# Performance work log

Hardware: AMD Instinct MI355X
Metric: run time of the kernel (lower is better)

The kernel has to match this reference:

```python
import jax, jax.numpy as jnp
import numpy as np

TEMPERATURE = 0.6
REPETITION_PENALTY = 1.2
VOCAB = 50257


def setup_inputs() -> dict:
    key = jax.random.key(0)
    k1, k2 = jax.random.split(key)
    logits = jax.random.normal(k1, (8, 64, VOCAB), dtype=jnp.float32)
    prev_tokens = jax.random.randint(k2, (64, 200), 0, VOCAB, dtype=jnp.int64)
    return {"logits": logits, "prev_tokens": prev_tokens}


def reference(logits, prev_tokens):
    # logits: [B, S, V]; prev_tokens: [S, P] token ids previously generated per sequence.
    B, S, V = logits.shape
    # set-semantics mask of penalized (seq, token) pairs; duplicate ids collapse to one.
    mask = jnp.zeros((S, V), dtype=bool).at[
        jnp.arange(S)[:, None], prev_tokens
    ].set(True)  # [S, V]
    # torch.all over dim 0: penalty multiplies if all batch logits negative, else divides.
    all_neg = jnp.all(logits < 0, axis=0, keepdims=True)  # [1, S, V]
    penalized = jnp.where(all_neg, logits * REPETITION_PENALTY, logits / REPETITION_PENALTY)
    logits = jnp.where(mask[None, :, :], penalized, logits)
    # Categorical(logits=x) -> probs = softmax(x); temperature scaling fused.
    return jax.nn.softmax(logits / TEMPERATURE, axis=-1)
```

## Files before the change

kernel.cpp:

```cpp
#include <hip/hip_runtime.h>
#include <math.h>

#define BB 8
#define SS 64
#define VV 50257
#define PP 200
#define NMASK 1571
#define NT 1024
#define ITER 13
constexpr float RP   = 1.2f;
constexpr float TINV = 1.0f / 0.6f;

__global__ __launch_bounds__(NT) void sch_fused_kernel(
        const float* __restrict__ logits,
        const int*   __restrict__ prev,
        float*       __restrict__ out) {
    __shared__ unsigned mask[NMASK];
    __shared__ float ss[16];
    __shared__ float bc_li;

    const int bs  = blockIdx.x;
    const int s   = bs & (SS - 1);
    const int tid = threadIdx.x;
    const float* row  = logits + (size_t)bs * VV;
    float*       orow = out    + (size_t)bs * VV;

    for (int i = tid; i < NMASK; i += NT) mask[i] = 0u;
    __syncthreads();

    float delta  = 0.0f;
    float eadj   = 0.0f;
    int   vtok   = -1;
    bool  winner = false;
    if (tid < PP) {
        vtok = prev[s * PP + tid];
        unsigned bit = 1u << (vtok & 31);
        unsigned old = atomicOr(&mask[vtok >> 5], bit);
        winner = (old & bit) == 0u;
        if (winner) {
            float lv[BB];
            bool all_neg = true;
            #pragma unroll
            for (int b = 0; b < BB; ++b) {
                lv[b] = logits[((size_t)(b * SS + s)) * VV + vtok];
                all_neg = all_neg && (lv[b] < 0.0f);
            }
            const float myraw = lv[bs >> 6];
            const float adj   = all_neg ? myraw * RP : myraw / RP;
            eadj  = __expf(adj * TINV);
            delta = eadj - __expf(myraw * TINV);
        }
    }

    const int a0   = (4 - (bs & 3)) & 3;
    const int nb   = (VV - a0) >> 2;
    const int tail = VV - a0 - (nb << 2);
    const int tstart = a0 + (nb << 2);

    const float4* body = (const float4*)(row + a0);
    float4 buf[ITER];
    #pragma unroll
    for (int k = 0; k < ITER; ++k) {
        int i = tid + k * NT;
        if (i < nb) buf[k] = body[i];
    }
    float escal = 0.0f;
    const bool has_head = (tid < a0);
    const bool has_tail = (tid >= 4 && tid < 4 + tail);
    if (has_head) escal = __expf(row[tid] * TINV);
    if (has_tail) escal = __expf(row[tstart + tid - 4] * TINV);

    float4 acc = make_float4(0.f, 0.f, 0.f, 0.f);
    #pragma unroll
    for (int k = 0; k < ITER; ++k) {
        int i = tid + k * NT;
        if (i < nb) {
            float4 x = buf[k];
            float4 e;
            e.x = __expf(x.x * TINV);
            e.y = __expf(x.y * TINV);
            e.z = __expf(x.z * TINV);
            e.w = __expf(x.w * TINV);
            buf[k] = e;
            acc.x += e.x; acc.y += e.y; acc.z += e.z; acc.w += e.w;
        }
    }
    float sum = (acc.x + acc.y) + (acc.z + acc.w) + escal + delta;

    #pragma unroll
    for (int off = 1; off < 64; off <<= 1)
        sum += __shfl_xor(sum, off);
    const int wave = tid >> 6, lane = tid & 63;
    if (lane == 0) ss[wave] = sum;
    __syncthreads();
    if (tid == 0) {
        float S0 = ss[0];
        #pragma unroll
        for (int w = 1; w < 16; ++w) S0 += ss[w];
        bc_li = 1.0f / S0;
    }
    __syncthreads();
    const float li = bc_li;

    float4* obody = (float4*)(orow + a0);
    #pragma unroll
    for (int k = 0; k < ITER; ++k) {
        int i = tid + k * NT;
        if (i < nb) {
            float4 e = buf[k];
            obody[i] = make_float4(e.x * li, e.y * li, e.z * li, e.w * li);
        }
    }
    if (has_head) orow[tid]               = escal * li;
    if (has_tail) orow[tstart + tid - 4]  = escal * li;

    __syncthreads();
    if (winner) orow[vtok] = eadj * li;
}

extern "C" void kernel_launch(void* const* d_in, const int* in_sizes, int n_in,
                              void* d_out, int out_size, void* d_ws, size_t ws_size,
                              hipStream_t stream) {
    const float* logits = (const float*)d_in[0];
    const int*   prev   = (const int*)d_in[1];
    float* out = (float*)d_out;

    sch_fused_kernel<<<BB * SS, NT, 0, stream>>>(logits, prev, out);
}
```

Baseline: 187.5 us.

## Process two rows per block, overlapping row0 normalization with row1 sum

```diff
diff --git a/kernel.cpp b/kernel.cpp
--- a/kernel.cpp
+++ b/kernel.cpp
@@ -7,31 +7,51 @@
 #define PP 200
 #define NMASK 1571
 #define NT 1024
-#define ITER 13
 constexpr float RP   = 1.2f;
 constexpr float TINV = 1.0f / 0.6f;
 
-__global__ __launch_bounds__(NT) void sch_fused_kernel(
+__device__ __forceinline__ float block_sum_recip(float v, int tid,
+                                                 float* swork, float* bc) {
+    #pragma unroll
+    for (int off = 1; off < 64; off <<= 1) v += __shfl_xor(v, off);
+    const int wave = tid >> 6, lane = tid & 63;
+    __syncthreads();
+    if (lane == 0) swork[wave] = v;
+    __syncthreads();
+    if (tid == 0) {
+        float S = swork[0];
+        #pragma unroll
+        for (int w = 1; w < 16; ++w) S += swork[w];
+        *bc = 1.0f / S;
+    }
+    __syncthreads();
+    return *bc;
+}
+
+__global__ __launch_bounds__(NT) void sch_pipe_kernel(
         const float* __restrict__ logits,
         const int*   __restrict__ prev,
         float*       __restrict__ out) {
     __shared__ unsigned mask[NMASK];
-    __shared__ float ss[16];
-    __shared__ float bc_li;
+    __shared__ float swork[16];
+    __shared__ float bc0, bc1;
 
-    const int bs  = blockIdx.x;
-    const int s   = bs & (SS - 1);
+    const int b   = blockIdx.x;
+    const int s   = b & (SS - 1);
     const int tid = threadIdx.x;
-    const float* row  = logits + (size_t)bs * VV;
-    float*       orow = out    + (size_t)bs * VV;
+    const int r0  = b;
+    const int r1  = b + 256;
+    const float* row0 = logits + (size_t)r0 * VV;
+    const float* row1 = logits + (size_t)r1 * VV;
+    float* orow0 = out + (size_t)r0 * VV;
+    float* orow1 = out + (size_t)r1 * VV;
 
     for (int i = tid; i < NMASK; i += NT) mask[i] = 0u;
     __syncthreads();
 
-    float delta  = 0.0f;
-    float eadj   = 0.0f;
-    int   vtok   = -1;
-    bool  winner = false;
+    float delta0 = 0.f, delta1 = 0.f, eadj0 = 0.f, eadj1 = 0.f;
+    int  vtok   = -1;
+    bool winner = false;
     if (tid < PP) {
         vtok = prev[s * PP + tid];
         unsigned bit = 1u << (vtok & 31);
@@ -41,81 +61,84 @@
             float lv[BB];
             bool all_neg = true;
             #pragma unroll
-            for (int b = 0; b < BB; ++b) {
-                lv[b] = logits[((size_t)(b * SS + s)) * VV + vtok];
-                all_neg = all_neg && (lv[b] < 0.0f);
+            for (int bb = 0; bb < BB; ++bb) {
+                lv[bb] = logits[((size_t)(bb * SS + s)) * VV + vtok];
+                all_neg = all_neg && (lv[bb] < 0.0f);
             }
-            const float myraw = lv[bs >> 6];
-            const float adj   = all_neg ? myraw * RP : myraw / RP;
-            eadj  = __expf(adj * TINV);
-            delta = eadj - __expf(myraw * TINV);
+            const int bat0 = b >> 6;
+            const float raw0 = lv[bat0];
+            const float raw1 = lv[bat0 + 4];
+            const float adj0 = all_neg ? raw0 * RP : raw0 / RP;
+            const float adj1 = all_neg ? raw1 * RP : raw1 / RP;
+            eadj0  = __expf(adj0 * TINV);
+            eadj1  = __expf(adj1 * TINV);
+            delta0 = eadj0 - __expf(raw0 * TINV);
+            delta1 = eadj1 - __expf(raw1 * TINV);
         }
     }
 
-    const int a0   = (4 - (bs & 3)) & 3;
+    const int a0   = (4 - (b & 3)) & 3;
     const int nb   = (VV - a0) >> 2;
     const int tail = VV - a0 - (nb << 2);
     const int tstart = a0 + (nb << 2);
-
-    const float4* body = (const float4*)(row + a0);
-    float4 buf[ITER];
-    #pragma unroll
-    for (int k = 0; k < ITER; ++k) {
-        int i = tid + k * NT;
-        if (i < nb) buf[k] = body[i];
-    }
-    float escal = 0.0f;
     const bool has_head = (tid < a0);
     const bool has_tail = (tid >= 4 && tid < 4 + tail);
-    if (has_head) escal = __expf(row[tid] * TINV);
-    if (has_tail) escal = __expf(row[tstart + tid - 4] * TINV);
 
-    float4 acc = make_float4(0.f, 0.f, 0.f, 0.f);
-    #pragma unroll
-    for (int k = 0; k < ITER; ++k) {
-        int i = tid + k * NT;
-        if (i < nb) {
-            float4 x = buf[k];
-            float4 e;
-            e.x = __expf(x.x * TINV);
-            e.y = __expf(x.y * TINV);
-            e.z = __expf(x.z * TINV);
-            e.w = __expf(x.w * TINV);
-            buf[k] = e;
-            acc.x += e.x; acc.y += e.y; acc.z += e.z; acc.w += e.w;
-        }
+    const float4* body0  = (const float4*)(row0 + a0);
+    const float4* body1  = (const float4*)(row1 + a0);
+    float4*       obody0 = (float4*)(orow0 + a0);
+    float4*       obody1 = (float4*)(orow1 + a0);
+
+    float sum0 = delta0;
+    for (int i = tid; i < nb; i += NT) {
+        float4 x = body0[i];
+        sum0 += (__expf(x.x * TINV) + __expf(x.y * TINV))
+              + (__expf(x.z * TINV) + __expf(x.w * TINV));
     }
-    float sum = (acc.x + acc.y) + (acc.z + acc.w) + escal + delta;
+    if (has_head) sum0 += __expf(row0[tid] * TINV);
+    if (has_tail) sum0 += __expf(row0[tstart + tid - 4] * TINV);
+    const float li0 = block_sum_recip(sum0, tid, swork, &bc0);
 
-    #pragma unroll
-    for (int off = 1; off < 64; off <<= 1)
-        sum += __shfl_xor(sum, off);
-    const int wave = tid >> 6, lane = tid & 63;
-    if (lane == 0) ss[wave] = sum;
-    __syncthreads();
-    if (tid == 0) {
-        float S0 = ss[0];
-        #pragma unroll
-        for (int w = 1; w < 16; ++w) S0 += ss[w];
-        bc_li = 1.0f / S0;
+    float sum1 = delta1;
+    for (int i = tid; i < nb; i += NT) {
+        float4 x0 = body0[i];
+        float4 x1 = body1[i];
+        float4 o;
+        o.x = __expf(x0.x * TINV) * li0;
+        o.y = __expf(x0.y * TINV) * li0;
+        o.z = __expf(x0.z * TINV) * li0;
+        o.w = __expf(x0.w * TINV) * li0;
+        obody0[i] = o;
+        sum1 += (__expf(x1.x * TINV) + __expf(x1.y * TINV))
+              + (__expf(x1.z * TINV) + __expf(x1.w * TINV));
     }
-    __syncthreads();
-    const float li = bc_li;
+    if (has_head) {
+        orow0[tid] = __expf(row0[tid] * TINV) * li0;
+        sum1 += __expf(row1[tid] * TINV);
+    }
+    if (has_tail) {
+        orow0[tstart + tid - 4] = __expf(row0[tstart + tid - 4] * TINV) * li0;
+        sum1 += __expf(row1[tstart + tid - 4] * TINV);
+    }
+    const float li1 = block_sum_recip(sum1, tid, swork, &bc1);
 
-    float4* obody = (float4*)(orow + a0);
-    #pragma unroll
-    for (int k = 0; k < ITER; ++k) {
-        int i = tid + k * NT;
-        if (i < nb) {
-            float4 e = buf[k];
-            obody[i] = make_float4(e.x * li, e.y * li, e.z * li, e.w * li);
-        }
+    for (int i = tid; i < nb; i += NT) {
+        float4 x1 = body1[i];
+        float4 o;
+        o.x = __expf(x1.x * TINV) * li1;
+        o.y = __expf(x1.y * TINV) * li1;
+        o.z = __expf(x1.z * TINV) * li1;
+        o.w = __expf(x1.w * TINV) * li1;
+        obody1[i] = o;
     }
-    if (has_head) orow[tid]               = escal * li;
-    if (has_tail) orow[tstart + tid - 4]  = escal * li;
+    if (has_head) orow1[tid]              = __expf(row1[tid] * TINV) * li1;
+    if (has_tail) orow1[tstart + tid - 4] = __expf(row1[tstart + tid - 4] * TINV) * li1;
 
     __syncthreads();
-    if (winner) orow[vtok] = eadj * li;
+    if (winner) {
+        orow0[vtok] = eadj0 * li0;
+        orow1[vtok] = eadj1 * li1;
+    }
 }
 
 extern "C" void kernel_launch(void* const* d_in, const int* in_sizes, int n_in,
@@ -125,5 +148,5 @@
     const int*   prev   = (const int*)d_in[1];
     float* out = (float*)d_out;
 
-    sch_fused_kernel<<<BB * SS, NT, 0, stream>>>(logits, prev, out);
+    sch_pipe_kernel<<<256, NT, 0, stream>>>(logits, prev, out);
 }
```

After: 196.9 us. 5.1% more time.

## Split fused softmax into four kernels with quarter-row parallelism

Applied to the files above, without the earlier changes.

```diff
diff --git a/kernel.cpp b/kernel.cpp
--- a/kernel.cpp
+++ b/kernel.cpp
@@ -6,116 +6,151 @@
 #define VV 50257
 #define PP 200
 #define NMASK 1571
-#define NT 1024
-#define ITER 13
+#define QQ 4
 constexpr float RP   = 1.2f;
 constexpr float TINV = 1.0f / 0.6f;
 
-__global__ __launch_bounds__(NT) void sch_fused_kernel(
-        const float* __restrict__ logits,
-        const int*   __restrict__ prev,
-        float*       __restrict__ out) {
+typedef float vfloat4 __attribute__((ext_vector_type(4)));
+
+
+__device__ __forceinline__ void row_geom(int r, int& a0, int& nb, int& tail) {
+    a0   = (4 - (r & 3)) & 3;
+    nb   = (VV - a0) >> 2;
+    tail = VV - a0 - (nb << 2);
+}
+
+__global__ __launch_bounds__(256) void k1_sums(const float* __restrict__ logits,
+                                               float* __restrict__ partials) {
+    const int j = blockIdx.x, r = j >> 2, q = j & 3, tid = threadIdx.x;
+    int a0, nb, tail; row_geom(r, a0, nb, tail);
+    const float* row = logits + (size_t)r * VV;
+    const float4* body = (const float4*)(row + a0);
+
+    const int nbq   = (nb + QQ - 1) >> 2;
+    const int start = q * nbq;
+    const int end   = min(nb, start + nbq);
+
+    float sum = 0.0f;
+    for (int i = start + tid; i < end; i += 256) {
+        float4 x = body[i];
+        sum += (__expf(x.x * TINV) + __expf(x.y * TINV))
+             + (__expf(x.z * TINV) + __expf(x.w * TINV));
+    }
+    if (q == 0 && tid < a0) sum += __expf(row[tid] * TINV);
+    const int tstart = a0 + (nb << 2);
+    if (q == 3 && tid >= 4 && tid < 4 + tail)
+        sum += __expf(row[tstart + tid - 4] * TINV);
+
+    #pragma unroll
+    for (int off = 1; off < 64; off <<= 1) sum += __shfl_xor(sum, off);
+    __shared__ float sw[4];
+    if ((tid & 63) == 0) sw[tid >> 6] = sum;
+    __syncthreads();
+    if (tid == 0) partials[j] = (sw[0] + sw[1]) + (sw[2] + sw[3]);
+}
+
+__global__ __launch_bounds__(256) void k2_corr(const float* __restrict__ logits,
+                                               const int*   __restrict__ prev,
+                                               const float* __restrict__ partials,
+                                               float*       __restrict__ li_inv) {
     __shared__ unsigned mask[NMASK];
-    __shared__ float ss[16];
-    __shared__ float bc_li;
+    __shared__ float deltas[BB];
+    const int s = blockIdx.x, tid = threadIdx.x;
 
-    const int bs  = blockIdx.x;
-    const int s   = bs & (SS - 1);
-    const int tid = threadIdx.x;
-    const float* row  = logits + (size_t)bs * VV;
-    float*       orow = out    + (size_t)bs * VV;
-
-    for (int i = tid; i < NMASK; i += NT) mask[i] = 0u;
+    for (int i = tid; i < NMASK; i += 256) mask[i] = 0u;
+    if (tid < BB) deltas[tid] = 0.0f;
     __syncthreads();
 
-    float delta  = 0.0f;
-    float eadj   = 0.0f;
-    int   vtok   = -1;
-    bool  winner = false;
     if (tid < PP) {
-        vtok = prev[s * PP + tid];
-        unsigned bit = 1u << (vtok & 31);
-        unsigned old = atomicOr(&mask[vtok >> 5], bit);
-        winner = (old & bit) == 0u;
-        if (winner) {
+        const int v = prev[s * PP + tid];
+        unsigned bit = 1u << (v & 31);
+        unsigned old = atomicOr(&mask[v >> 5], bit);
+        if ((old & bit) == 0u) {
             float lv[BB];
             bool all_neg = true;
             #pragma unroll
             for (int b = 0; b < BB; ++b) {
-                lv[b] = logits[((size_t)(b * SS + s)) * VV + vtok];
+                lv[b] = logits[((size_t)(b * SS + s)) * VV + v];
                 all_neg = all_neg && (lv[b] < 0.0f);
             }
-            const float myraw = lv[bs >> 6];
-            const float adj   = all_neg ? myraw * RP : myraw / RP;
-            eadj  = __expf(adj * TINV);
-            delta = eadj - __expf(myraw * TINV);
+            #pragma unroll
+            for (int b = 0; b < BB; ++b) {
+                const float adj = all_neg ? lv[b] * RP : lv[b] / RP;
+                atomicAdd(&deltas[b], __expf(adj * TINV) - __expf(lv[b] * TINV));
+            }
         }
     }
+    __syncthreads();
+    if (tid < BB) {
+        const int bs = tid * SS + s;
+        const float S = (partials[bs * 4 + 0] + partials[bs * 4 + 1])
+                      + (partials[bs * 4 + 2] + partials[bs * 4 + 3]);
+        li_inv[bs] = 1.0f / (S + deltas[tid]);
+    }
+}
 
-    const int a0   = (4 - (bs & 3)) & 3;
-    const int nb   = (VV - a0) >> 2;
-    const int tail = VV - a0 - (nb << 2);
+__global__ __launch_bounds__(256) void k3_write(const float* __restrict__ logits,
+                                                const float* __restrict__ li_inv,
+                                                float* __restrict__ out) {
+    const int j = blockIdx.x, r = j >> 2, q = j & 3, tid = threadIdx.x;
+    int a0, nb, tail; row_geom(r, a0, nb, tail);
+    const float* row  = logits + (size_t)r * VV;
+    float*       orow = out    + (size_t)r * VV;
+    const float4* body  = (const float4*)(row + a0);
+    vfloat4*      obody = (vfloat4*)(orow + a0);
+    const float li = li_inv[r];
+
+    const int nbq   = (nb + QQ - 1) >> 2;
+    const int start = q * nbq;
+    const int end   = min(nb, start + nbq);
+
+    for (int i = start + tid; i < end; i += 256) {
+        float4 x = body[i];
+        vfloat4 o;
+        o.x = __expf(x.x * TINV) * li;
+        o.y = __expf(x.y * TINV) * li;
+        o.z = __expf(x.z * TINV) * li;
+        o.w = __expf(x.w * TINV) * li;
+        __builtin_nontemporal_store(o, &obody[i]);
+    }
+    if (q == 0 && tid < a0)
+        __builtin_nontemporal_store(__expf(row[tid] * TINV) * li, &orow[tid]);
     const int tstart = a0 + (nb << 2);
+    if (q == 3 && tid >= 4 && tid < 4 + tail)
+        __builtin_nontemporal_store(__expf(row[tstart + tid - 4] * TINV) * li,
+                                    &orow[tstart + tid - 4]);
+}
 
-    const float4* body = (const float4*)(row + a0);
-    float4 buf[ITER];
-    #pragma unroll
-    for (int k = 0; k < ITER; ++k) {
-        int i = tid + k * NT;
-        if (i < nb) buf[k] = body[i];
-    }
-    float escal = 0.0f;
-    const bool has_head = (tid < a0);
-    const bool has_tail = (tid >= 4 && tid < 4 + tail);
-    if (has_head) escal = __expf(row[tid] * TINV);
-    if (has_tail) escal = __expf(row[tstart + tid - 4] * TINV);
+__global__ __launch_bounds__(256) void k4_fix(const float* __restrict__ logits,
+                                              const int*   __restrict__ prev,
+                                              const float* __restrict__ li_inv,
+                                              float* __restrict__ out) {
+    __shared__ unsigned mask[NMASK];
+    const int s = blockIdx.x, tid = threadIdx.x;
 
-    float4 acc = make_float4(0.f, 0.f, 0.f, 0.f);
-    #pragma unroll
-    for (int k = 0; k < ITER; ++k) {
-        int i = tid + k * NT;
-        if (i < nb) {
-            float4 x = buf[k];
-            float4 e;
-            e.x = __expf(x.x * TINV);
-            e.y = __expf(x.y * TINV);
-            e.z = __expf(x.z * TINV);
-            e.w = __expf(x.w * TINV);
-            buf[k] = e;
-            acc.x += e.x; acc.y += e.y; acc.z += e.z; acc.w += e.w;
+    for (int i = tid; i < NMASK; i += 256) mask[i] = 0u;
+    __syncthreads();
+
+    if (tid < PP) {
+        const int v = prev[s * PP + tid];
+        unsigned bit = 1u << (v & 31);
+        unsigned old = atomicOr(&mask[v >> 5], bit);
+        if ((old & bit) == 0u) {
+            float lv[BB];
+            bool all_neg = true;
+            #pragma unroll
+            for (int b = 0; b < BB; ++b) {
+                lv[b] = logits[((size_t)(b * SS + s)) * VV + v];
+                all_neg = all_neg && (lv[b] < 0.0f);
+            }
+            #pragma unroll
+            for (int b = 0; b < BB; ++b) {
+                const int bs = b * SS + s;
+                const float adj = all_neg ? lv[b] * RP : lv[b] / RP;
+                out[(size_t)bs * VV + v] = __expf(adj * TINV) * li_inv[bs];
+            }
         }
     }
-    float sum = (acc.x + acc.y) + (acc.z + acc.w) + escal + delta;
-
-    #pragma unroll
-    for (int off = 1; off < 64; off <<= 1)
-        sum += __shfl_xor(sum, off);
-    const int wave = tid >> 6, lane = tid & 63;
-    if (lane == 0) ss[wave] = sum;
-    __syncthreads();
-    if (tid == 0) {
-        float S0 = ss[0];
-        #pragma unroll
-        for (int w = 1; w < 16; ++w) S0 += ss[w];
-        bc_li = 1.0f / S0;
-    }
-    __syncthreads();
-    const float li = bc_li;
-
-    float4* obody = (float4*)(orow + a0);
-    #pragma unroll
-    for (int k = 0; k < ITER; ++k) {
-        int i = tid + k * NT;
-        if (i < nb) {
-            float4 e = buf[k];
-            obody[i] = make_float4(e.x * li, e.y * li, e.z * li, e.w * li);
-        }
-    }
-    if (has_head) orow[tid]               = escal * li;
-    if (has_tail) orow[tstart + tid - 4]  = escal * li;
-
-    __syncthreads();
-    if (winner) orow[vtok] = eadj * li;
 }
 
 extern "C" void kernel_launch(void* const* d_in, const int* in_sizes, int n_in,
@@ -125,5 +160,11 @@
     const int*   prev   = (const int*)d_in[1];
     float* out = (float*)d_out;
 
-    sch_fused_kernel<<<BB * SS, NT, 0, stream>>>(logits, prev, out);
+    float* partials = (float*)d_ws;
+    float* li_inv   = partials + 512 * QQ;
+
+    k1_sums <<<512 * QQ, 256, 0, stream>>>(logits, partials);
+    k2_corr <<<SS,       256, 0, stream>>>(logits, prev, partials, li_inv);
+    k3_write<<<512 * QQ, 256, 0, stream>>>(logits, li_inv, out);
+    k4_fix  <<<SS,       256, 0, stream>>>(logits, prev, li_inv, out);
 }
```

New measurement: 234.5 us. +25.1%, slower.
